# Kernel optimization log

Measured on AMD Instinct MI355X. Metric: run time of the kernel, lower is better.

Reference implementation:

```python
import jax, jax.numpy as jnp
import numpy as np

BEAMS = (1, 3, 1, 5, 1)
DIM_CAT, DIM_SOL, DIM_RG, H, M = 54, 87, 235, 1024, 256
BATCH = 8192


def setup_inputs():
    key = jax.random.key(0)
    keys = iter(jax.random.split(key, 96))
    s = 0.02

    def lin(din, dout):
        return (jax.random.normal(next(keys), (din, dout), jnp.float32) * s,
                jax.random.normal(next(keys), (dout,), jnp.float32) * s)

    inp = {"features": jax.random.normal(next(keys), (BATCH, H), jnp.float32)}
    inp["Wc"], inp["bc"] = lin(DIM_CAT, M)
    inp["Ws1"], inp["bs1"] = lin(DIM_SOL, M)
    inp["Ws2"], inp["bs2"] = lin(DIM_SOL, M)
    inp["Wr"], inp["br"] = lin(DIM_RG, M)
    outs = (DIM_CAT, DIM_SOL, DIM_SOL, DIM_RG, DIM_RG)
    for i in range(5):
        inp["Wh1_%d" % i], inp["bh1_%d" % i] = lin(H + i * M, H)
        inp["Wh2_%d" % i], inp["bh2_%d" % i] = lin(H, H)
        inp["Wo_%d" % i], inp["bo_%d" % i] = lin(H, outs[i])
    return inp


def _beam_search(features, in_params, hid_params):
    # Vectorized equivalent of the python beam loops: all combinatorial beam
    # indices of a stage are folded into one batched MLP pass.
    b0, b1, b2, b3, b4 = BEAMS
    B = features.shape[0]

    def msg(oh, j):  # one-hot [B,n,D] -> message [B,n,M]  (self.inputs[j])
        W, b = in_params[j]
        return jax.nn.relu(oh @ W + b)

    def stage(i, msgs, n, k):
        feat = jnp.broadcast_to(features[:, None, :], (B, n, H))
        x = jnp.concatenate([feat] + msgs, axis=-1)
        Wh1, bh1, Wh2, bh2, Wo, bo = hid_params[i]
        h = jax.nn.relu(x @ Wh1 + bh1)
        h = jnp.tanh(h @ Wh2 + bh2)
        p = jax.nn.softmax(h @ Wo + bo, axis=-1)
        sc, ix = jax.lax.top_k(p, k)  # [B,n,k]
        return sc.reshape(B, n * k), ix.reshape(B, n * k)

    s0, i0 = stage(0, [], 1, b0)
    oh0 = jax.nn.one_hot(i0, DIM_CAT, dtype=features.dtype)

    s1, i1 = stage(1, [msg(oh0, 0)], b0, b1)
    oh1 = jax.nn.one_hot(i1, DIM_SOL, dtype=features.dtype)

    n2 = b0 * b1
    ix = jnp.arange(n2)
    s2, i2 = stage(2, [msg(oh0[:, ix // b1], 0), msg(oh1[:, ix], 1)], n2, b2)
    oh2 = jax.nn.one_hot(i2, DIM_SOL, dtype=features.dtype)

    n3 = n2 * b2
    ix = jnp.arange(n3)
    s3, i3 = stage(3, [msg(oh0[:, ix // (b1 * b2)], 0),
                       msg(oh1[:, ix // b2], 1),
                       msg(oh2[:, ix], 2)], n3, b3)
    oh3 = jax.nn.one_hot(i3, DIM_RG, dtype=features.dtype)

    n4 = n3 * b3
    ix = jnp.arange(n4)
    s4, i4 = stage(4, [msg(oh0[:, ix // (b1 * b2 * b3)], 0),
                       msg(oh1[:, ix // (b2 * b3)], 1),
                       msg(oh2[:, ix // b3], 2),
                       msg(oh3[:, ix], 3)], n4, b4)

    # expansion factors (== torch .repeat(...).reshape pattern)
    f = (b1 * b2 * b3 * b4, b2 * b3 * b4, b3 * b4, b4)
    rep = lambda a, r: jnp.repeat(a, r, axis=1)
    topk = jnp.stack([rep(i0, f[0]), rep(i1, f[1]), rep(i2, f[2]),
                      rep(i3, f[3]), i4], axis=-1)  # [B,K,5]
    score = rep(s0, f[0]) * rep(s1, f[1]) * rep(s2, f[2]) * rep(s3, f[3]) * s4
    order = jnp.argsort(-score, axis=-1)  # descending sort of joint scores
    score_sorted = jnp.take_along_axis(score, order, axis=-1)
    topk = jnp.take_along_axis(topk, order[..., None], axis=1)
    return topk, score_sorted


def reference(features, Wc, bc, Ws1, bs1, Ws2, bs2, Wr, br,
              Wh1_0, bh1_0, Wh2_0, bh2_0, Wo_0, bo_0,
              Wh1_1, bh1_1, Wh2_1, bh2_1, Wo_1, bo_1,
              Wh1_2, bh1_2, Wh2_2, bh2_2, Wo_2, bo_2,
              Wh1_3, bh1_3, Wh2_3, bh2_3, Wo_3, bo_3,
              Wh1_4, bh1_4, Wh2_4, bh2_4, Wo_4, bo_4):
    in_params = [(Wc, bc), (Ws1, bs1), (Ws2, bs2), (Wr, br)]
    hid_params = [
        (Wh1_0, bh1_0, Wh2_0, bh2_0, Wo_0, bo_0),
        (Wh1_1, bh1_1, Wh2_1, bh2_1, Wo_1, bo_1),
        (Wh1_2, bh1_2, Wh2_2, bh2_2, Wo_2, bo_2),
        (Wh1_3, bh1_3, Wh2_3, bh2_3, Wo_3, bo_3),
        (Wh1_4, bh1_4, Wh2_4, bh2_4, Wo_4, bo_4),
    ]
    topk, _ = _beam_search(features, in_params, hid_params)
    return topk
```

## Files before the change

kernel.cpp:

```cpp
#include <hip/hip_runtime.h>
#include <math.h>

#define NB 8192
enum { ACT_NONE = 0, ACT_RELU = 1, ACT_TANH = 2 };

typedef double d4_t __attribute__((ext_vector_type(4)));

struct GSet {
    const float* T;
    const float* bT;
    const int*   idx;
    int is, io;
};

template<typename TA, int ACT, bool HB, bool HA>
__global__ __launch_bounds__(256)
void mgemm3(const TA* __restrict__ A, int lda, int KA,
            const float* __restrict__ W,
            const float* __restrict__ bias,
            const double* __restrict__ addsrc,
            double* __restrict__ C, int K,
            GSet g0, GSet g1)
{
    __shared__ double Al[16][129];
    __shared__ double Bl[16][128];
    __shared__ int idc[2][128];
    const int tid  = threadIdx.x;
    const int lane = tid & 63;
    const int w    = tid >> 6;
    const int q    = lane >> 4;
    const int c    = lane & 15;
    const int m0w  = (w >> 1) * 64;
    const int n0w  = (w & 1) * 64;
    const size_t m0 = (size_t)blockIdx.y * 128;
    const int    n0 = blockIdx.x * 128;

    const int srow = tid >> 1;
    const int half = tid & 1;
    const int bk   = tid >> 4;
    const int bseg = tid & 15;

    const int ns = (K - KA) >> 8;
    if (ns > 0 && tid < 128)
        idc[0][tid] = g0.idx[(size_t)(m0 + tid) * g0.is + g0.io];
    if (ns > 1 && tid >= 128)
        idc[1][tid - 128] = g1.idx[(size_t)(m0 + tid - 128) * g1.is + g1.io];

    d4_t acc[4][4];
#pragma unroll
    for (int i = 0; i < 4; i++)
#pragma unroll
        for (int j = 0; j < 4; j++) acc[i][j] = (d4_t){0.0, 0.0, 0.0, 0.0};

    __syncthreads();

    for (int kt = 0; kt < K; kt += 16) {
        {
            const int kb = kt + half * 8;
            if (kb < KA) {
                const TA* ap = A + (m0 + srow) * (size_t)lda + kb;
#pragma unroll
                for (int e = 0; e < 8; e++)
                    Al[half * 8 + e][srow] = (double)ap[e];
            } else {
                const int koff = kb - KA;
                const int s = koff >> 8;
                const int lk = koff & 255;
                const GSet& g = s ? g1 : g0;
                const float* tp = g.T + (size_t)idc[s][srow] * 256 + lk;
                const float* bp = g.bT + lk;
#pragma unroll
                for (int e = 0; e < 8; e++) {
                    double v = (double)tp[e] + (double)bp[e];
                    Al[half * 8 + e][srow] = v > 0.0 ? v : 0.0;
                }
            }
        }
        {
            const float* wp = W + (size_t)(kt + bk) * 1024 + n0 + bseg;
#pragma unroll
            for (int e = 0; e < 8; e++)
                Bl[bk][bseg + 16 * e] = (double)wp[16 * e];
        }
        __syncthreads();
#pragma unroll
        for (int kk = 0; kk < 4; kk++) {
            double a[4], b[4];
#pragma unroll
            for (int i = 0; i < 4; i++) a[i] = Al[kk * 4 + q][m0w + i * 16 + c];
#pragma unroll
            for (int j = 0; j < 4; j++) b[j] = Bl[kk * 4 + q][n0w + j * 16 + c];
#pragma unroll
            for (int i = 0; i < 4; i++)
#pragma unroll
                for (int j = 0; j < 4; j++)
                    acc[i][j] = __builtin_amdgcn_mfma_f64_16x16x4f64(
                        a[i], b[j], acc[i][j], 0, 0, 0);
        }
        __syncthreads();
    }

#pragma unroll
    for (int i = 0; i < 4; i++)
#pragma unroll
        for (int j = 0; j < 4; j++)
#pragma unroll
            for (int v = 0; v < 4; v++) {
                size_t gr = m0 + m0w + i * 16 + q * 4 + v;
                int    gc = n0 + n0w + j * 16 + c;
                double val = acc[i][j][v];
                if (HB) val += (double)bias[gc];
                if (HA) val += addsrc[gr * 1024 + gc];
                if (ACT == ACT_RELU) val = val > 0.0 ? val : 0.0;
                if (ACT == ACT_TANH) val = tanh(val);
                C[gr * 1024 + gc] = val;
            }
}

__global__ __launch_bounds__(256)
void wo_topk(const double* __restrict__ h2,
             const float* __restrict__ W, const float* __restrict__ bo,
             int N, int k,
             float* __restrict__ sout, int* __restrict__ iout,
             int stride, int soff)
{
    __shared__ double h2s[8][1024];
    __shared__ double dred[256];
    __shared__ float  pred[256];
    __shared__ int    ired[256];
    const int tid = threadIdx.x;
    const size_t rbase = (size_t)blockIdx.x * 8;

    for (int t = tid; t < 8192; t += 256)
        h2s[t >> 10][t & 1023] = h2[(rbase + (t >> 10)) * 1024 + (t & 1023)];
    __syncthreads();

    const int c = tid;
    double a[8] = {0, 0, 0, 0, 0, 0, 0, 0};
    if (c < N) {
        for (int kk = 0; kk < 1024; kk++) {
            double wv = (double)W[(size_t)kk * N + c];
#pragma unroll
            for (int r = 0; r < 8; r++)
                a[r] = fma(h2s[r][kk], wv, a[r]);
        }
    }
    double bb = (c < N) ? (double)bo[c] : 0.0;

    for (int r = 0; r < 8; r++) {
        size_t b = rbase + r;
        double lgv = a[r] + bb;
        dred[tid] = (c < N) ? lgv : -INFINITY;
        __syncthreads();
        for (int s = 128; s; s >>= 1) {
            if (tid < s) dred[tid] = fmax(dred[tid], dred[tid + s]);
            __syncthreads();
        }
        double mx = dred[0];
        __syncthreads();
        double e = (c < N) ? exp(lgv - mx) : 0.0;
        dred[tid] = e;
        __syncthreads();
        for (int s = 128; s; s >>= 1) {
            if (tid < s) dred[tid] += dred[tid + s];
            __syncthreads();
        }
        double se = dred[0];
        __syncthreads();
        float p = (c < N) ? (float)(e / se) : -1.f;

        for (int kk = 0; kk < k; kk++) {
            pred[tid] = p;
            ired[tid] = (c < N) ? c : (1 << 20);
            __syncthreads();
            for (int s = 128; s; s >>= 1) {
                if (tid < s) {
                    float ov = pred[tid + s]; int oi = ired[tid + s];
                    if (ov > pred[tid] || (ov == pred[tid] && oi < ired[tid])) {
                        pred[tid] = ov; ired[tid] = oi;
                    }
                }
                __syncthreads();
            }
            if (tid == 0) {
                sout[b * stride + soff + kk] = pred[0];
                iout[b * stride + soff + kk] = ired[0];
            }
            int win = ired[0];
            __syncthreads();
            if (c == win) p = -1.f;
        }
    }
}

__global__ void finalize_q(const float* __restrict__ s0, const float* __restrict__ s1,
                           const float* __restrict__ s2, const float* __restrict__ s3,
                           const float* __restrict__ s4,
                           const int* __restrict__ i0, const int* __restrict__ i1,
                           const int* __restrict__ i2, const int* __restrict__ i3,
                           const int* __restrict__ i4,
                           int* __restrict__ out)
{
    int b = blockIdx.x * 256 + threadIdx.x;
    float sc[15];
    float a0 = s0[b];
    for (int t = 0; t < 15; t++) {
        int a = t / 5;
        float v = a0 * s1[b * 3 + a];
        v = v * s2[b * 3 + a];
        v = v * s3[b * 15 + t];
        v = v * s4[b * 15 + t];
        sc[t] = v;
    }
    bool used[15] = {false};
    for (int r = 0; r < 15; r++) {
        int best = -1; float bv = -INFINITY;
        for (int t = 0; t < 15; t++)
            if (!used[t] && sc[t] > bv) { bv = sc[t]; best = t; }
        used[best] = true;
        int a = best / 5;
        int* o = out + (size_t)b * 75 + r * 5;
        o[0] = i0[b];
        o[1] = i1[b * 3 + a];
        o[2] = i2[b * 3 + a];
        o[3] = i3[b * 15 + best];
        o[4] = i4[b * 15 + best];
    }
}

static const GSet GNULL = {nullptr, nullptr, nullptr, 0, 0};

static void mm(hipStream_t st, int a_is_f32, const void* A, int lda, int KA,
               const float* W, const float* bias,
               const double* add, double* C, int K, int rows,
               GSet g0, GSet g1, int act)
{
    dim3 grid(8, rows / 128);
#define LK(TA, AC, HBv, HAv) hipLaunchKernelGGL((mgemm3<TA, AC, HBv, HAv>), grid, dim3(256), 0, st, \
        (const TA*)A, lda, KA, W, bias, add, C, K, g0, g1)
#define ACTS(TA, HBv, HAv) do { if (act == 0) LK(TA, 0, HBv, HAv); \
                                else if (act == 1) LK(TA, 1, HBv, HAv); \
                                else LK(TA, 2, HBv, HAv); } while (0)
#define BDISP(TA) do { if (bias) { if (add) ACTS(TA, true, true); else ACTS(TA, true, false); } \
                       else      { if (add) ACTS(TA, false, true); else ACTS(TA, false, false); } } while (0)
    if (a_is_f32) BDISP(float); else BDISP(double);
#undef BDISP
#undef ACTS
#undef LK
}

extern "C" void kernel_launch(void* const* d_in, const int* in_sizes, int n_in,
                              void* d_out, int out_size, void* d_ws, size_t ws_size,
                              hipStream_t stream)
{
    (void)in_sizes; (void)n_in; (void)out_size;
    const float* feat = (const float*)d_in[0];
    const float* Wc  = (const float*)d_in[1];
    const float* bc  = (const float*)d_in[2];
    const float* Ws1 = (const float*)d_in[3];
    const float* bs1 = (const float*)d_in[4];
    const float* Ws2 = (const float*)d_in[5];
    const float* bs2 = (const float*)d_in[6];
    const float* Wr  = (const float*)d_in[7];
    const float* br  = (const float*)d_in[8];
    auto Wh1 = [&](int i) { return (const float*)d_in[9 + 6 * i]; };
    auto bh1 = [&](int i) { return (const float*)d_in[10 + 6 * i]; };
    auto Wh2 = [&](int i) { return (const float*)d_in[11 + 6 * i]; };
    auto bh2 = [&](int i) { return (const float*)d_in[12 + 6 * i]; };
    auto Wo  = [&](int i) { return (const float*)d_in[13 + 6 * i]; };
    auto bo  = [&](int i) { return (const float*)d_in[14 + 6 * i]; };
    const int outs[5] = {54, 87, 87, 235, 235};

    const size_t perRow = 4096ull * 8 + 37ull * 4 + 37ull * 4;
    int R = NB;
    while (R > 1024 && (size_t)R * perRow > ws_size) R >>= 1;

    double* ws = (double*)d_ws;
    size_t off = 0;
    auto alloc = [&](size_t n) { double* p = ws + off; off += n; return p; };
    double* bufC = alloc((size_t)R * 1024);
    double* base = alloc((size_t)R * 1024);
    double* h1   = alloc((size_t)R * 1024);
    double* h2   = alloc((size_t)R * 1024);
    float* fbase = (float*)(ws + off);
    float* s0 = fbase;            float* s1 = fbase + R;
    float* s2 = s1 + 3 * R;       float* s3 = s2 + 3 * R;
    float* s4 = s3 + 15 * R;
    int* ibase = (int*)(s4 + 15 * R);
    int* i0 = ibase;              int* i1 = ibase + R;
    int* i2 = i1 + 3 * R;         int* i3 = i2 + 3 * R;
    int* i4 = i3 + 15 * R;

    for (int r0 = 0; r0 < NB; r0 += R) {
        const float* fC = feat + (size_t)r0 * 1024;
        auto WOT = [&](int st, int N, int k, float* so, int* io_, int stride, int soff) {
            hipLaunchKernelGGL(wo_topk, dim3(R / 8), dim3(256), 0, stream,
                               h2, Wo(st), bo(st), N, k, so, io_, stride, soff);
        };

        mm(stream, 1, fC, 1024, 1024, Wh1(0), bh1(0), nullptr, h1, 1024, R, GNULL, GNULL, ACT_RELU);
        mm(stream, 0, h1, 1024, 1024, Wh2(0), bh2(0), nullptr, h2, 1024, R, GNULL, GNULL, ACT_TANH);
        WOT(0, outs[0], 1, s0, i0, 1, 0);

        GSet gm0 = {Wc, bc, i0, 1, 0};

        mm(stream, 1, fC, 1024, 1024, Wh1(1), bh1(1), nullptr, h1, 1280, R, gm0, GNULL, ACT_RELU);
        mm(stream, 0, h1, 1024, 1024, Wh2(1), bh2(1), nullptr, h2, 1024, R, GNULL, GNULL, ACT_TANH);
        WOT(1, outs[1], 3, s1, i1, 3, 0);

        mm(stream, 1, fC, 1024, 1024, Wh1(2), nullptr, nullptr, bufC, 1280, R, gm0, GNULL, ACT_NONE);
        for (int a = 0; a < 3; a++) {
            GSet g = {Ws1, bs1, i1, 3, a};
            mm(stream, 1, nullptr, 0, 0, Wh1(2) + (size_t)1280 * 1024, bh1(2), bufC, h1, 256, R, g, GNULL, ACT_RELU);
            mm(stream, 0, h1, 1024, 1024, Wh2(2), bh2(2), nullptr, h2, 1024, R, GNULL, GNULL, ACT_TANH);
            WOT(2, outs[2], 1, s2, i2, 3, a);
        }

        mm(stream, 1, fC, 1024, 1024, Wh1(3), nullptr, nullptr, bufC, 1280, R, gm0, GNULL, ACT_NONE);
        for (int a = 0; a < 3; a++) {
            GSet ga = {Ws1, bs1, i1, 3, a};
            GSet gb = {Ws2, bs2, i2, 3, a};
            mm(stream, 1, nullptr, 0, 0, Wh1(3) + (size_t)1280 * 1024, bh1(3), bufC, h1, 512, R, ga, gb, ACT_RELU);
            mm(stream, 0, h1, 1024, 1024, Wh2(3), bh2(3), nullptr, h2, 1024, R, GNULL, GNULL, ACT_TANH);
            WOT(3, outs[3], 5, s3, i3, 15, 5 * a);
        }

        mm(stream, 1, fC, 1024, 1024, Wh1(4), nullptr, nullptr, bufC, 1280, R, gm0, GNULL, ACT_NONE);
        for (int a = 0; a < 3; a++) {
            GSet ga = {Ws1, bs1, i1, 3, a};
            GSet gb = {Ws2, bs2, i2, 3, a};
            mm(stream, 1, nullptr, 0, 0, Wh1(4) + (size_t)1280 * 1024, nullptr, bufC, base, 512, R, ga, gb, ACT_NONE);
            for (int cc = 0; cc < 5; cc++) {
                int t = a * 5 + cc;
                GSet gr_ = {Wr, br, i3, 15, t};
                mm(stream, 1, nullptr, 0, 0, Wh1(4) + (size_t)1792 * 1024, bh1(4), base, h1, 256, R, gr_, GNULL, ACT_RELU);
                mm(stream, 0, h1, 1024, 1024, Wh2(4), bh2(4), nullptr, h2, 1024, R, GNULL, GNULL, ACT_TANH);
                WOT(4, outs[4], 1, s4, i4, 15, t);
            }
        }

        hipLaunchKernelGGL(finalize_q, dim3(R / 256), dim3(256), 0, stream,
                           s0, s1, s2, s3, s4, i0, i1, i2, i3, i4, (int*)d_out + (size_t)r0 * 75);
    }
}
```

Baseline: 22.50 ms.

## Fuse stage-4 beam loop into persistent cooperative kernel with grid barriers

```diff
diff --git a/kernel.cpp b/kernel.cpp
--- a/kernel.cpp
+++ b/kernel.cpp
@@ -13,7 +13,7 @@
     int is, io;
 };
 
-template<typename TA, int ACT, bool HB, bool HA>
+template<typename TA, int ACT, bool HB, bool HA, int NS>
 __global__ __launch_bounds__(256)
 void mgemm3(const TA* __restrict__ A, int lda, int KA,
             const float* __restrict__ W,
@@ -40,10 +40,9 @@
     const int bk   = tid >> 4;
     const int bseg = tid & 15;
 
-    const int ns = (K - KA) >> 8;
-    if (ns > 0 && tid < 128)
+    if (NS > 0 && tid < 128)
         idc[0][tid] = g0.idx[(size_t)(m0 + tid) * g0.is + g0.io];
-    if (ns > 1 && tid >= 128)
+    if (NS > 1 && tid >= 128)
         idc[1][tid - 128] = g1.idx[(size_t)(m0 + tid - 128) * g1.is + g1.io];
 
     d4_t acc[4][4];
@@ -52,10 +51,15 @@
 #pragma unroll
         for (int j = 0; j < 4; j++) acc[i][j] = (d4_t){0.0, 0.0, 0.0, 0.0};
 
-    __syncthreads();
+    if (NS > 0) __syncthreads();
 
     for (int kt = 0; kt < K; kt += 16) {
-        {
+        if (NS == 0) {
+            const TA* ap = A + (m0 + srow) * (size_t)lda + kt + half * 8;
+#pragma unroll
+            for (int e = 0; e < 8; e++)
+                Al[half * 8 + e][srow] = (double)ap[e];
+        } else {
             const int kb = kt + half * 8;
             if (kb < KA) {
                 const TA* ap = A + (m0 + srow) * (size_t)lda + kb;
@@ -228,6 +232,233 @@
     }
 }
 
+union SM {
+    struct { double Al[16][129]; double Bl[16][128]; int idc[2][128]; } g;
+    struct { double h2s[8][1024]; double dred[256]; float pred[256]; int ired[256]; } t;
+};
+
+struct S4Args {
+    const double* bufC; double* base; double* h1; double* h2;
+    const float* W4a; const float* W4b;
+    const float* bh1_4; const float* Wh2_4; const float* bh2_4;
+    const float* Wo4; const float* bo4;
+    const float* Ws1; const float* bs1; const float* Ws2; const float* bs2;
+    const float* Wr;  const float* br;
+    const int* i1; const int* i2; const int* i3;
+    float* s4; int* i4;
+    unsigned* bar;
+    int nblk;
+};
+
+__device__ __forceinline__ void grid_bar(unsigned* bar, int nblk)
+{
+    __threadfence();
+    __syncthreads();
+    if (threadIdx.x == 0) {
+        unsigned g = __atomic_load_n(&bar[1], __ATOMIC_ACQUIRE);
+        unsigned v = __atomic_add_fetch(&bar[0], 1u, __ATOMIC_ACQ_REL);
+        if (v == (unsigned)nblk) {
+            __atomic_store_n(&bar[0], 0u, __ATOMIC_RELAXED);
+            __atomic_store_n(&bar[1], g + 1u, __ATOMIC_RELEASE);
+        } else {
+            while (__atomic_load_n(&bar[1], __ATOMIC_ACQUIRE) == g)
+                __builtin_amdgcn_s_sleep(8);
+        }
+    }
+    __syncthreads();
+    __threadfence();
+}
+
+template<int ACT, bool HB, bool HA, int NS, bool AHEAD>
+__device__ __forceinline__ void gphase(SM* sm,
+    const double* __restrict__ A,
+    const float* __restrict__ W,
+    const float* __restrict__ bias,
+    const double* __restrict__ addsrc,
+    double* __restrict__ C, int K,
+    GSet g0, GSet g1)
+{
+    const int tid  = threadIdx.x;
+    const int lane = tid & 63;
+    const int w    = tid >> 6;
+    const int q    = lane >> 4;
+    const int c    = lane & 15;
+    const int m0w  = (w >> 1) * 64;
+    const int n0w  = (w & 1) * 64;
+    const size_t m0 = (size_t)(blockIdx.x >> 3) * 128;
+    const int    n0 = (blockIdx.x & 7) * 128;
+
+    const int srow = tid >> 1;
+    const int half = tid & 1;
+    const int bk   = tid >> 4;
+    const int bseg = tid & 15;
+
+    if (!AHEAD) {
+        if (NS > 0 && tid < 128)
+            sm->g.idc[0][tid] = g0.idx[(size_t)(m0 + tid) * g0.is + g0.io];
+        if (NS > 1 && tid >= 128)
+            sm->g.idc[1][tid - 128] = g1.idx[(size_t)(m0 + tid - 128) * g1.is + g1.io];
+    }
+
+    d4_t acc[4][4];
+#pragma unroll
+    for (int i = 0; i < 4; i++)
+#pragma unroll
+        for (int j = 0; j < 4; j++) acc[i][j] = (d4_t){0.0, 0.0, 0.0, 0.0};
+
+    if (!AHEAD) __syncthreads();
+
+    for (int kt = 0; kt < K; kt += 16) {
+        if (AHEAD) {
+            const double* ap = A + (m0 + srow) * 1024 + kt + half * 8;
+#pragma unroll
+            for (int e = 0; e < 8; e++)
+                sm->g.Al[half * 8 + e][srow] = ap[e];
+        } else {
+            const int koff = kt + half * 8;
+            const int s = koff >> 8;
+            const int lk = koff & 255;
+            const GSet& g = (NS > 1 && s) ? g1 : g0;
+            const float* tp = g.T + (size_t)sm->g.idc[s][srow] * 256 + lk;
+            const float* bp = g.bT + lk;
+#pragma unroll
+            for (int e = 0; e < 8; e++) {
+                double v = (double)tp[e] + (double)bp[e];
+                sm->g.Al[half * 8 + e][srow] = v > 0.0 ? v : 0.0;
+            }
+        }
+        {
+            const float* wp = W + (size_t)(kt + bk) * 1024 + n0 + bseg;
+#pragma unroll
+            for (int e = 0; e < 8; e++)
+                sm->g.Bl[bk][bseg + 16 * e] = (double)wp[16 * e];
+        }
+        __syncthreads();
+#pragma unroll
+        for (int kk = 0; kk < 4; kk++) {
+            double a[4], b[4];
+#pragma unroll
+            for (int i = 0; i < 4; i++) a[i] = sm->g.Al[kk * 4 + q][m0w + i * 16 + c];
+#pragma unroll
+            for (int j = 0; j < 4; j++) b[j] = sm->g.Bl[kk * 4 + q][n0w + j * 16 + c];
+#pragma unroll
+            for (int i = 0; i < 4; i++)
+#pragma unroll
+                for (int j = 0; j < 4; j++)
+                    acc[i][j] = __builtin_amdgcn_mfma_f64_16x16x4f64(
+                        a[i], b[j], acc[i][j], 0, 0, 0);
+        }
+        __syncthreads();
+    }
+
+#pragma unroll
+    for (int i = 0; i < 4; i++)
+#pragma unroll
+        for (int j = 0; j < 4; j++)
+#pragma unroll
+            for (int v = 0; v < 4; v++) {
+                size_t gr = m0 + m0w + i * 16 + q * 4 + v;
+                int    gc = n0 + n0w + j * 16 + c;
+                double val = acc[i][j][v];
+                if (HB) val += (double)bias[gc];
+                if (HA) val += addsrc[gr * 1024 + gc];
+                if (ACT == ACT_RELU) val = val > 0.0 ? val : 0.0;
+                if (ACT == ACT_TANH) val = tanh(val);
+                C[gr * 1024 + gc] = val;
+            }
+}
+
+__device__ __forceinline__ void wophase(SM* sm,
+    const double* __restrict__ h2,
+    const float* __restrict__ W, const float* __restrict__ bo,
+    int N, float* __restrict__ sout, int* __restrict__ iout,
+    int stride, int soff)
+{
+    const int tid = threadIdx.x;
+    for (int grp = 0; grp < 2; grp++) {
+        const size_t rbase = (size_t)blockIdx.x * 16 + grp * 8;
+        for (int t = tid; t < 8192; t += 256)
+            sm->t.h2s[t >> 10][t & 1023] = h2[(rbase + (t >> 10)) * 1024 + (t & 1023)];
+        __syncthreads();
+
+        const int c = tid;
+        double a[8] = {0, 0, 0, 0, 0, 0, 0, 0};
+        if (c < N) {
+            for (int kk = 0; kk < 1024; kk++) {
+                double wv = (double)W[(size_t)kk * N + c];
+#pragma unroll
+                for (int r = 0; r < 8; r++)
+                    a[r] = fma(sm->t.h2s[r][kk], wv, a[r]);
+            }
+        }
+        double bb = (c < N) ? (double)bo[c] : 0.0;
+
+        for (int r = 0; r < 8; r++) {
+            size_t b = rbase + r;
+            double lgv = a[r] + bb;
+            sm->t.dred[tid] = (c < N) ? lgv : -INFINITY;
+            __syncthreads();
+            for (int s = 128; s; s >>= 1) {
+                if (tid < s) sm->t.dred[tid] = fmax(sm->t.dred[tid], sm->t.dred[tid + s]);
+                __syncthreads();
+            }
+            double mx = sm->t.dred[0];
+            __syncthreads();
+            double e = (c < N) ? exp(lgv - mx) : 0.0;
+            sm->t.dred[tid] = e;
+            __syncthreads();
+            for (int s = 128; s; s >>= 1) {
+                if (tid < s) sm->t.dred[tid] += sm->t.dred[tid + s];
+                __syncthreads();
+            }
+            double se = sm->t.dred[0];
+            __syncthreads();
+            float p = (c < N) ? (float)(e / se) : -1.f;
+
+            sm->t.pred[tid] = p;
+            sm->t.ired[tid] = (c < N) ? c : (1 << 20);
+            __syncthreads();
+            for (int s = 128; s; s >>= 1) {
+                if (tid < s) {
+                    float ov = sm->t.pred[tid + s]; int oi = sm->t.ired[tid + s];
+                    if (ov > sm->t.pred[tid] || (ov == sm->t.pred[tid] && oi < sm->t.ired[tid])) {
+                        sm->t.pred[tid] = ov; sm->t.ired[tid] = oi;
+                    }
+                }
+                __syncthreads();
+            }
+            if (tid == 0) {
+                sout[b * stride + soff] = sm->t.pred[0];
+                iout[b * stride + soff] = sm->t.ired[0];
+            }
+            __syncthreads();
+        }
+        __syncthreads();
+    }
+}
+
+__global__ __launch_bounds__(256, 2)
+void s4persist(S4Args p)
+{
+    __shared__ SM sm;
+    for (int a = 0; a < 3; a++) {
+        GSet ga = {p.Ws1, p.bs1, p.i1, 3, a};
+        GSet gb = {p.Ws2, p.bs2, p.i2, 3, a};
+        gphase<ACT_NONE, false, true, 2, false>(&sm, nullptr, p.W4a, nullptr, p.bufC, p.base, 512, ga, gb);
+        grid_bar(p.bar, p.nblk);
+        for (int cc = 0; cc < 5; cc++) {
+            int t = a * 5 + cc;
+            GSet gr_ = {p.Wr, p.br, p.i3, 15, t};
+            gphase<ACT_RELU, true, true, 1, false>(&sm, nullptr, p.W4b, p.bh1_4, p.base, p.h1, 256, gr_, gr_);
+            grid_bar(p.bar, p.nblk);
+            gphase<ACT_TANH, true, false, 0, true>(&sm, p.h1, p.Wh2_4, p.bh2_4, nullptr, p.h2, 1024, gr_, gr_);
+            grid_bar(p.bar, p.nblk);
+            wophase(&sm, p.h2, p.Wo4, p.bo4, 235, p.s4, p.i4, 15, t);
+            grid_bar(p.bar, p.nblk);
+        }
+    }
+}
+
 static const GSet GNULL = {nullptr, nullptr, nullptr, 0, 0};
 
 static void mm(hipStream_t st, int a_is_f32, const void* A, int lda, int KA,
@@ -236,16 +467,21 @@
                GSet g0, GSet g1, int act)
 {
     dim3 grid(8, rows / 128);
-#define LK(TA, AC, HBv, HAv) hipLaunchKernelGGL((mgemm3<TA, AC, HBv, HAv>), grid, dim3(256), 0, st, \
+    int ns = (K - KA) >> 8;
+#define LK(TA, AC, HBv, HAv, NSv) hipLaunchKernelGGL((mgemm3<TA, AC, HBv, HAv, NSv>), grid, dim3(256), 0, st, \
         (const TA*)A, lda, KA, W, bias, add, C, K, g0, g1)
-#define ACTS(TA, HBv, HAv) do { if (act == 0) LK(TA, 0, HBv, HAv); \
-                                else if (act == 1) LK(TA, 1, HBv, HAv); \
-                                else LK(TA, 2, HBv, HAv); } while (0)
+#define NSD(TA, AC, HBv, HAv) do { if (ns == 0) LK(TA, AC, HBv, HAv, 0); \
+                                   else if (ns == 1) LK(TA, AC, HBv, HAv, 1); \
+                                   else LK(TA, AC, HBv, HAv, 2); } while (0)
+#define ACTS(TA, HBv, HAv) do { if (act == 0) NSD(TA, 0, HBv, HAv); \
+                                else if (act == 1) NSD(TA, 1, HBv, HAv); \
+                                else NSD(TA, 2, HBv, HAv); } while (0)
 #define BDISP(TA) do { if (bias) { if (add) ACTS(TA, true, true); else ACTS(TA, true, false); } \
                        else      { if (add) ACTS(TA, false, true); else ACTS(TA, false, false); } } while (0)
     if (a_is_f32) BDISP(float); else BDISP(double);
 #undef BDISP
 #undef ACTS
+#undef NSD
 #undef LK
 }
 
@@ -273,7 +509,7 @@
 
     const size_t perRow = 4096ull * 8 + 37ull * 4 + 37ull * 4;
     int R = NB;
-    while (R > 1024 && (size_t)R * perRow > ws_size) R >>= 1;
+    while (R > 1024 && (size_t)R * perRow + 256 > ws_size) R >>= 1;
 
     double* ws = (double*)d_ws;
     size_t off = 0;
@@ -290,6 +526,7 @@
     int* i0 = ibase;              int* i1 = ibase + R;
     int* i2 = i1 + 3 * R;         int* i3 = i2 + 3 * R;
     int* i4 = i3 + 15 * R;
+    unsigned* bar = (unsigned*)(i4 + 15 * R);
 
     for (int r0 = 0; r0 < NB; r0 += R) {
         const float* fC = feat + (size_t)r0 * 1024;
@@ -326,16 +563,29 @@
         }
 
         mm(stream, 1, fC, 1024, 1024, Wh1(4), nullptr, nullptr, bufC, 1280, R, gm0, GNULL, ACT_NONE);
-        for (int a = 0; a < 3; a++) {
-            GSet ga = {Ws1, bs1, i1, 3, a};
-            GSet gb = {Ws2, bs2, i2, 3, a};
-            mm(stream, 1, nullptr, 0, 0, Wh1(4) + (size_t)1280 * 1024, nullptr, bufC, base, 512, R, ga, gb, ACT_NONE);
-            for (int cc = 0; cc < 5; cc++) {
-                int t = a * 5 + cc;
-                GSet gr_ = {Wr, br, i3, 15, t};
-                mm(stream, 1, nullptr, 0, 0, Wh1(4) + (size_t)1792 * 1024, bh1(4), base, h1, 256, R, gr_, GNULL, ACT_RELU);
-                mm(stream, 0, h1, 1024, 1024, Wh2(4), bh2(4), nullptr, h2, 1024, R, GNULL, GNULL, ACT_TANH);
-                WOT(4, outs[4], 1, s4, i4, 15, t);
+        {
+            hipMemsetAsync(bar, 0, 128, stream);
+            S4Args args = {bufC, base, h1, h2,
+                           Wh1(4) + (size_t)1280 * 1024, Wh1(4) + (size_t)1792 * 1024,
+                           bh1(4), Wh2(4), bh2(4), Wo(4), bo(4),
+                           Ws1, bs1, Ws2, bs2, Wr, br,
+                           i1, i2, i3, s4, i4, bar, 8 * (R / 128)};
+            void* kp[] = {&args};
+            hipError_t ce = hipLaunchCooperativeKernel((void*)s4persist,
+                                dim3(8 * (R / 128)), dim3(256), kp, 0, stream);
+            if (ce != hipSuccess) {
+                for (int a = 0; a < 3; a++) {
+                    GSet ga = {Ws1, bs1, i1, 3, a};
+                    GSet gb = {Ws2, bs2, i2, 3, a};
+                    mm(stream, 1, nullptr, 0, 0, Wh1(4) + (size_t)1280 * 1024, nullptr, bufC, base, 512, R, ga, gb, ACT_NONE);
+                    for (int cc = 0; cc < 5; cc++) {
+                        int t = a * 5 + cc;
+                        GSet gr_ = {Wr, br, i3, 15, t};
+                        mm(stream, 1, nullptr, 0, 0, Wh1(4) + (size_t)1792 * 1024, bh1(4), base, h1, 256, R, gr_, GNULL, ACT_RELU);
+                        mm(stream, 0, h1, 1024, 1024, Wh2(4), bh2(4), nullptr, h2, 1024, R, GNULL, GNULL, ACT_TANH);
+                        WOT(4, outs[4], 1, s4, i4, 15, t);
+                    }
+                }
             }
         }
 
```

New measurement: 43.86 ms. 1.95x slower.
